# Performance work log

Measured on AMD Instinct MI355X. Metric: run time of the kernel, lower is better.

Reference implementation:

```python
import jax, jax.numpy as jnp
import numpy as np

N = 100000      # nodes
E = 400000      # edges (before self loops)
D_ATOM = 98
D_BOND = 13
EMB = 128
HEADS = 4
L = 4           # num_layer


def prelu(x, a):
    return jnp.where(x >= 0, x, a * x)


def setup_inputs() -> dict:
    key = jax.random.key(0)
    ks = jax.random.split(key, 12)
    s = 0.05
    inp = {
        "x": jax.random.normal(ks[0], (N, D_ATOM), dtype=jnp.float32),
        "edge_index": jax.random.randint(ks[1], (2, E), 0, N, dtype=jnp.int64),
        "edge_attr": jax.random.uniform(ks[2], (E, D_BOND), dtype=jnp.float32),
        # GNN-level params
        "x_emb_W": jax.random.normal(ks[3], (D_ATOM, EMB), dtype=jnp.float32) * s,
        "prelu_gnn": jnp.float32(0.25),
        # per-layer GATConv params, stacked on leading layer axis
        "wl_W": jax.random.normal(ks[4], (L, EMB, HEADS * EMB), dtype=jnp.float32) * s,
        "wl_b": jnp.zeros((L, HEADS * EMB), dtype=jnp.float32),
        "att": jax.random.normal(ks[5], (L, HEADS, 2 * EMB), dtype=jnp.float32) * s,
        "gat_bias": jnp.zeros((L, EMB), dtype=jnp.float32),
        "ee_W": jax.random.normal(ks[6], (L, D_BOND, HEADS * EMB), dtype=jnp.float32) * s,
        "ee_b": jnp.zeros((L, HEADS * EMB), dtype=jnp.float32),
        "prelu_gat": jnp.full((L,), 0.25, dtype=jnp.float32),
        # LayerNorm params per layer
        "ln_g": jnp.ones((L, EMB), dtype=jnp.float32),
        "ln_b": jnp.zeros((L, EMB), dtype=jnp.float32),
    }
    return inp


def reference(x, edge_index, edge_attr, x_emb_W, prelu_gnn, wl_W, wl_b, att,
              gat_bias, ee_W, ee_b, prelu_gat, ln_g, ln_b):
    # add self loops: (i, i) for every node; self-loop edge_attr = zeros
    loop = jnp.arange(N, dtype=edge_index.dtype)
    src = jnp.concatenate([edge_index[0], loop])  # [E+N] source (j)
    dst = jnp.concatenate([edge_index[1], loop])  # [E+N] target (i)
    ea = jnp.concatenate(
        [edge_attr, jnp.zeros((N, D_BOND), dtype=edge_attr.dtype)], axis=0)

    # input embedding + shared PReLU
    h = prelu(x @ x_emb_W, prelu_gnn)  # [N, EMB]

    for l in range(L):
        a = prelu_gat[l]
        ee = prelu(ea @ ee_W[l] + ee_b[l], a)       # [E+N, H*EMB]
        xw = prelu(h @ wl_W[l] + wl_b[l], a)        # [N, H*EMB]
        x_i = xw[dst].reshape(-1, HEADS, EMB)       # target feats
        x_j = (xw[src] + ee).reshape(-1, HEADS, EMB)  # source feats + edge emb
        # attention logits: cat([x_i,x_j]) . att
        alpha = (x_i * att[l, :, :EMB]).sum(-1) + (x_j * att[l, :, EMB:]).sum(-1)
        alpha = prelu(alpha, a)                     # [E+N, HEADS]
        # segment softmax grouped by src (edge_index[0]), as in the module
        m = jax.ops.segment_max(alpha, src, num_segments=N)
        alpha = jnp.exp(alpha - m[src])
        ssum = jax.ops.segment_sum(alpha, src, num_segments=N)
        alpha = alpha / (ssum[src] + 1e-16)
        # weighted messages, scatter-add to target nodes
        msg = (x_j * alpha[:, :, None]).reshape(-1, HEADS * EMB)
        aggr = jax.ops.segment_sum(msg, dst, num_segments=N)
        aggr = aggr.reshape(N, HEADS, EMB).mean(axis=1) + gat_bias[l]
        # LayerNorm
        mu = aggr.mean(-1, keepdims=True)
        var = ((aggr - mu) ** 2).mean(-1, keepdims=True)
        hn = (aggr - mu) / jnp.sqrt(var + 1e-5) * ln_g[l] + ln_b[l]
        # dropout is identity (drop_ratio=0); PReLU on all but last layer
        h = hn if l == L - 1 else prelu(hn, prelu_gnn)

    return h  # JK='last'
```

## Files before the change

kernel.cpp:

```cpp
#include <hip/hip_runtime.h>
#include <stdint.h>

#define NN 100000
#define NE 400000
#define NT 500000
#define DA 98
#define DB 13
#define EMB 128
#define HE 512
#define NWAVE 8192
#define IMSK 0x0FFFFFFF

typedef unsigned short ushort_t;
typedef __bf16 bf16x8 __attribute__((ext_vector_type(8)));
typedef float floatx4 __attribute__((ext_vector_type(4)));
typedef __fp16 fp16v2 __attribute__((ext_vector_type(2)));

__device__ __forceinline__ float prelu_f(float x, float a) { return x >= 0.f ? x : a * x; }

__device__ __forceinline__ ushort_t f2bf(float f) {
    unsigned u = __float_as_uint(f);
    unsigned r = (u + 0x7fffu + ((u >> 16) & 1u)) >> 16;
    return (ushort_t)r;
}
__device__ __forceinline__ float bflo(unsigned u) { return __uint_as_float(u << 16); }
__device__ __forceinline__ float bfhi(unsigned u) { return __uint_as_float(u & 0xffff0000u); }

__device__ __forceinline__ float dot2(unsigned a, unsigned b, float c) {
    return __builtin_amdgcn_fdot2(__builtin_bit_cast(fp16v2, a), __builtin_bit_cast(fp16v2, b), c, false);
}

__device__ __forceinline__ unsigned pk2(float lo, float hi) {
    fp16v2 p = __builtin_amdgcn_cvt_pkrtz(lo, hi);
    return __builtin_bit_cast(unsigned, p);
}

__global__ void k_count(const int* __restrict__ ei, int* __restrict__ sc, int* __restrict__ dc) {
    int e = blockIdx.x * 256 + threadIdx.x;
    if (e >= NT) return;
    int s, d;
    if (e < NE) { s = ei[e]; d = ei[NE + e]; } else { s = d = e - NE; }
    atomicAdd(sc + s, 1);
    atomicAdd(dc + d, 1);
}

__global__ void k_scan1(const int* __restrict__ cnt, int* __restrict__ part, int* __restrict__ bsum) {
    __shared__ int tmp[512];
    int t = threadIdx.x, i = blockIdx.x * 512 + t;
    int v = (i < NN) ? cnt[i] : 0;
    tmp[t] = v;
    __syncthreads();
    for (int off = 1; off < 512; off <<= 1) {
        int x = (t >= off) ? tmp[t - off] : 0;
        __syncthreads();
        tmp[t] += x;
        __syncthreads();
    }
    if (i < NN) part[i] = tmp[t] - v;
    if (t == 511) bsum[blockIdx.x] = tmp[t];
}

__global__ void k_scan2(int* __restrict__ bsum, int nb) {
    __shared__ int tmp[256];
    int t = threadIdx.x;
    int v = (t < nb) ? bsum[t] : 0;
    tmp[t] = v;
    __syncthreads();
    for (int off = 1; off < 256; off <<= 1) {
        int x = (t >= off) ? tmp[t - off] : 0;
        __syncthreads();
        tmp[t] += x;
        __syncthreads();
    }
    if (t < nb) bsum[t] = tmp[t] - v;
}

__global__ void k_scan3(const int* __restrict__ part, const int* __restrict__ bsum,
                        int* __restrict__ off, int* __restrict__ cur) {
    int i = blockIdx.x * 256 + threadIdx.x;
    if (i < NN) {
        int v = part[i] + bsum[i >> 9];
        off[i] = v;
        cur[i] = v;
    }
    if (i == 0) off[NN] = NT;
}

__global__ void k_fill(const int* __restrict__ ei, int* __restrict__ scur, int* __restrict__ dcur,
                       int* __restrict__ seid, int* __restrict__ deid, int* __restrict__ s2p) {
    int e = blockIdx.x * 256 + threadIdx.x;
    if (e >= NT) return;
    int s, d;
    if (e < NE) { s = ei[e]; d = ei[NE + e]; } else { s = d = e - NE; }
    int p = atomicAdd(scur + s, 1);
    seid[p] = e;
    s2p[e] = p;
    deid[atomicAdd(dcur + d, 1)] = e;
}

__global__ void k_wrange2(const int* __restrict__ doff, const int* __restrict__ soff,
                          int* __restrict__ nstart, int* __restrict__ nstart_s) {
    int w = blockIdx.x * 256 + threadIdx.x;
    if (w > NWAVE) return;
    long long target = (long long)w * NT / NWAVE;
    int lo = 0, hi = NN;
    while (lo < hi) {
        int mid = (lo + hi) >> 1;
        if ((long long)doff[mid] < target) lo = mid + 1; else hi = mid;
    }
    nstart[w] = lo;
    lo = 0; hi = NN;
    while (lo < hi) {
        int mid = (lo + hi) >> 1;
        if ((long long)soff[mid] < target) lo = mid + 1; else hi = mid;
    }
    nstart_s[w] = lo;
}

__global__ void k_dprep(const int* __restrict__ deid, const int* __restrict__ ei,
                        const float* __restrict__ ea, const int* __restrict__ s2p,
                        int2* __restrict__ sd_d, unsigned* __restrict__ ea_d) {
    int i = blockIdx.x * 256 + threadIdx.x;
    if (i >= NT + 4) return;
    unsigned p[8] = {0, 0, 0, 0, 0, 0, 0, 0};
    int s = 0, pos = 0;
    if (i < NT) {
        int eid = deid[i];
        if (eid < NE) {
            s = ei[eid];
            float v[DB];
            #pragma unroll
            for (int k = 0; k < DB; ++k) v[k] = ea[(size_t)eid * DB + k];
            #pragma unroll
            for (int kp = 0; kp < 6; ++kp) p[kp] = pk2(v[2 * kp], v[2 * kp + 1]);
            p[6] = pk2(v[12], 0.f);
        } else {
            s = (eid - NE) | (1 << 30);
        }
        pos = s2p[eid];
    }
    uint4* o = (uint4*)&ea_d[(size_t)i * 8];
    o[0] = make_uint4(p[0], p[1], p[2], p[3]);
    o[1] = make_uint4(p[4], p[5], p[6], p[7]);
    sd_d[i] = make_int2(s, pos);
}

__global__ void k_sprep(const int* __restrict__ seid, const int* __restrict__ ei,
                        const float* __restrict__ ea,
                        int* __restrict__ dst_s, unsigned* __restrict__ ea_s) {
    int i = blockIdx.x * 256 + threadIdx.x;
    if (i >= NT + 4) return;
    unsigned p[8] = {0, 0, 0, 0, 0, 0, 0, 0};
    int d = 0;
    if (i < NT) {
        int eid = seid[i];
        if (eid < NE) {
            d = ei[NE + eid];
            float v[DB];
            #pragma unroll
            for (int k = 0; k < DB; ++k) v[k] = ea[(size_t)eid * DB + k];
            #pragma unroll
            for (int kp = 0; kp < 6; ++kp) p[kp] = pk2(v[2 * kp], v[2 * kp + 1]);
            p[6] = pk2(v[12], 0.f);
        } else {
            d = (eid - NE) | (1 << 30);
        }
    }
    uint4* o = (uint4*)&ea_s[(size_t)i * 8];
    o[0] = make_uint4(p[0], p[1], p[2], p[3]);
    o[1] = make_uint4(p[4], p[5], p[6], p[7]);
    dst_s[i] = d;
}

__global__ void k_prep_all(const float* __restrict__ x, const float* __restrict__ xembW,
                           const float* __restrict__ wlW, const float* __restrict__ eeW,
                           ushort_t* __restrict__ xb, ushort_t* __restrict__ Wxt,
                           ushort_t* __restrict__ Wtg, unsigned* __restrict__ eeWp) {
    int idx = blockIdx.x * 256 + threadIdx.x;
    if (idx < NN * 128) {
        int col = idx & 127, n = idx >> 7;
        float v = (col < DA) ? x[(size_t)n * DA + col] : 0.f;
        xb[idx] = f2bf(v);
        return;
    }
    idx -= NN * 128;
    if (idx < 128 * 128) {
        int k = idx & 127, n = idx >> 7;
        float v = (k < DA) ? xembW[(size_t)k * EMB + n] : 0.f;
        Wxt[idx] = f2bf(v);
        return;
    }
    idx -= 128 * 128;
    if (idx < 4 * 512 * 128) {
        int k = idx & 127;
        int n = (idx >> 7) & 511;
        int l = idx >> 16;
        Wtg[idx] = f2bf(wlW[(size_t)l * 65536 + k * 512 + n]);
        return;
    }
    idx -= 4 * 512 * 128;
    if (idx < 4 * 7 * 512) {
        int l = idx / 3584;
        int rem = idx - l * 3584;
        int kp = rem >> 9;
        int ch = rem & 511;
        float lo = eeW[((size_t)l * DB + 2 * kp) * HE + ch];
        float hi = (2 * kp + 1 < DB) ? eeW[((size_t)l * DB + 2 * kp + 1) * HE + ch] : 0.f;
        eeWp[idx] = pk2(lo, hi);
    }
}
#define PREP_TOTAL (NN * 128 + 128 * 128 + 4 * 512 * 128 + 4 * 7 * 512)

__global__ __launch_bounds__(256) void k_embed_m(const ushort_t* __restrict__ xb, const ushort_t* __restrict__ Wxt,
                                                 const float* __restrict__ pg, ushort_t* __restrict__ hb) {
    __shared__ ushort_t At[64 * 136];
    __shared__ ushort_t Bt[128 * 136];
    int t = threadIdx.x;
    int m0 = blockIdx.x * 64;
    for (int idx = t; idx < 64 * 16; idx += 256) {
        int r = idx >> 4, co = (idx & 15) * 8;
        int gr = m0 + r; if (gr >= NN) gr = 0;
        *(uint4*)&At[r * 136 + co] = *(const uint4*)&xb[(size_t)gr * 128 + co];
    }
    for (int idx = t; idx < 128 * 16; idx += 256) {
        int n = idx >> 4, ko = (idx & 15) * 8;
        *(uint4*)&Bt[n * 136 + ko] = *(const uint4*)&Wxt[n * 128 + ko];
    }
    float p = pg[0];
    __syncthreads();

    int wv = t >> 6, lane = t & 63;
    int ml = lane & 15, kq = lane >> 4;
    int n0w = wv * 32;
    floatx4 acc[4][2];
    #pragma unroll
    for (int mt = 0; mt < 4; ++mt)
        #pragma unroll
        for (int nt = 0; nt < 2; ++nt)
            acc[mt][nt] = (floatx4){0.f, 0.f, 0.f, 0.f};

    #pragma unroll
    for (int k0 = 0; k0 < 128; k0 += 32) {
        bf16x8 af[4], bfv[2];
        #pragma unroll
        for (int mt = 0; mt < 4; ++mt) {
            uint4 u = *(const uint4*)&At[(mt * 16 + ml) * 136 + k0 + kq * 8];
            af[mt] = __builtin_bit_cast(bf16x8, u);
        }
        #pragma unroll
        for (int nt = 0; nt < 2; ++nt) {
            uint4 u = *(const uint4*)&Bt[(n0w + nt * 16 + ml) * 136 + k0 + kq * 8];
            bfv[nt] = __builtin_bit_cast(bf16x8, u);
        }
        #pragma unroll
        for (int mt = 0; mt < 4; ++mt)
            #pragma unroll
            for (int nt = 0; nt < 2; ++nt)
                acc[mt][nt] = __builtin_amdgcn_mfma_f32_16x16x32_bf16(af[mt], bfv[nt], acc[mt][nt], 0, 0, 0);
    }
    #pragma unroll
    for (int nt = 0; nt < 2; ++nt) {
        int col = n0w + nt * 16 + ml;
        #pragma unroll
        for (int mt = 0; mt < 4; ++mt) {
            int row = m0 + mt * 16 + kq * 4;
            #pragma unroll
            for (int q = 0; q < 4; ++q) {
                int r = row + q;
                if (r < NN) hb[(size_t)r * EMB + col] = f2bf(prelu_f(acc[mt][nt][q], p));
            }
        }
    }
}

__global__ __launch_bounds__(256) void k_gemm(const ushort_t* __restrict__ hb, const ushort_t* __restrict__ Wtg,
                                              const float* __restrict__ bl, const float* __restrict__ pa,
                                              const float* __restrict__ attl,
                                              ushort_t* __restrict__ xw,
                                              float* __restrict__ ddst, float* __restrict__ dsrc) {
    __shared__ ushort_t At[64 * 136];
    __shared__ ushort_t Bt[128 * 136];
    int t = threadIdx.x;
    int m0 = blockIdx.x * 64;
    int h = blockIdx.y;
    int n0 = h * 128;
    for (int idx = t; idx < 64 * 16; idx += 256) {
        int r = idx >> 4, co = (idx & 15) * 8;
        int gr = m0 + r; if (gr >= NN) gr = 0;
        *(uint4*)&At[r * 136 + co] = *(const uint4*)&hb[(size_t)gr * EMB + co];
    }
    for (int idx = t; idx < 128 * 16; idx += 256) {
        int n = idx >> 4, ko = (idx & 15) * 8;
        *(uint4*)&Bt[n * 136 + ko] = *(const uint4*)&Wtg[(size_t)(n0 + n) * 128 + ko];
    }
    float a = pa[0];
    __syncthreads();

    int wv = t >> 6, lane = t & 63;
    int ml = lane & 15, kq = lane >> 4;
    int n0w = wv * 32;
    floatx4 acc[4][2];
    #pragma unroll
    for (int mt = 0; mt < 4; ++mt)
        #pragma unroll
        for (int nt = 0; nt < 2; ++nt)
            acc[mt][nt] = (floatx4){0.f, 0.f, 0.f, 0.f};

    #pragma unroll
    for (int k0 = 0; k0 < 128; k0 += 32) {
        bf16x8 af[4], bfv[2];
        #pragma unroll
        for (int mt = 0; mt < 4; ++mt) {
            uint4 u = *(const uint4*)&At[(mt * 16 + ml) * 136 + k0 + kq * 8];
            af[mt] = __builtin_bit_cast(bf16x8, u);
        }
        #pragma unroll
        for (int nt = 0; nt < 2; ++nt) {
            uint4 u = *(const uint4*)&Bt[(n0w + nt * 16 + ml) * 136 + k0 + kq * 8];
            bfv[nt] = __builtin_bit_cast(bf16x8, u);
        }
        #pragma unroll
        for (int mt = 0; mt < 4; ++mt)
            #pragma unroll
            for (int nt = 0; nt < 2; ++nt)
                acc[mt][nt] = __builtin_amdgcn_mfma_f32_16x16x32_bf16(af[mt], bfv[nt], acc[mt][nt], 0, 0, 0);
    }
    __syncthreads();
    float* sdd = (float*)At;
    float* sds = (float*)At + 256;

    float pd[4][4], ps[4][4];
    #pragma unroll
    for (int mt = 0; mt < 4; ++mt)
        #pragma unroll
        for (int q = 0; q < 4; ++q) { pd[mt][q] = 0.f; ps[mt][q] = 0.f; }

    #pragma unroll
    for (int nt = 0; nt < 2; ++nt) {
        int ch = n0w + nt * 16 + ml;
        int col = n0 + ch;
        float bv = bl[col];
        float a1v = attl[h * 256 + ch];
        float a2v = attl[h * 256 + 128 + ch];
        #pragma unroll
        for (int mt = 0; mt < 4; ++mt) {
            int row = m0 + mt * 16 + kq * 4;
            #pragma unroll
            for (int q = 0; q < 4; ++q) {
                int r = row + q;
                float v = prelu_f(acc[mt][nt][q] + bv, a);
                if (r < NN) xw[(size_t)r * HE + col] = f2bf(v);
                pd[mt][q] += v * a1v;
                ps[mt][q] += v * a2v;
            }
        }
    }
    #pragma unroll
    for (int mt = 0; mt < 4; ++mt)
        #pragma unroll
        for (int q = 0; q < 4; ++q) {
            float d = pd[mt][q], s = ps[mt][q];
            #pragma unroll
            for (int m = 1; m < 16; m <<= 1) {
                d += __shfl_xor(d, m, 64);
                s += __shfl_xor(s, m, 64);
            }
            if (ml == 0) {
                int lr = mt * 16 + kq * 4 + q;
                sdd[wv * 64 + lr] = d;
                sds[wv * 64 + lr] = s;
            }
        }
    __syncthreads();
    if (t < 64) {
        int r = m0 + t;
        if (r < NN) {
            float d = sdd[t] + sdd[64 + t] + sdd[128 + t] + sdd[192 + t];
            float s = sds[t] + sds[64 + t] + sds[128 + t] + sds[192 + t];
            ddst[r * 4 + h] = d;
            dsrc[r * 4 + h] = s;
        }
    }
}

__global__ __launch_bounds__(256) void k_edgesm(const int* __restrict__ nstart_s,
                                                const int* __restrict__ soff,
                                                const unsigned* __restrict__ ea_s,
                                                const int* __restrict__ dst_s,
                                                const unsigned* __restrict__ eeWp, const float* __restrict__ ebl,
                                                const float* __restrict__ attl, const float* __restrict__ pa,
                                                const float* __restrict__ ddst, const float* __restrict__ dsrc,
                                                float* __restrict__ alpha_s) {
    int t = threadIdx.x;
    float a = pa[0];
    int lane = t & 63;
    int w = blockIdx.x * 4 + (t >> 6);
    int hd = lane >> 4;
    int cm = (lane & 15) * 8;
    int c0 = lane * 8;
    uint4 wpa[7], wpb[7];
    #pragma unroll
    for (int kp = 0; kp < 7; ++kp) {
        wpa[kp] = *(const uint4*)&eeWp[kp * HE + c0];
        wpb[kp] = *(const uint4*)&eeWp[kp * HE + c0 + 4];
    }
    float a2[8], eb[8];
    #pragma unroll
    for (int q = 0; q < 8; ++q) {
        a2[q] = attl[hd * 256 + 128 + cm + q];
        eb[q] = ebl[c0 + q];
    }
    float pselfR = 0.f;
    #pragma unroll
    for (int q = 0; q < 8; ++q) pselfR += prelu_f(eb[q], a) * a2[q];
    #pragma unroll
    for (int m = 1; m < 16; m <<= 1) pselfR += __shfl_xor(pselfR, m, 64);

    int head = lane & 3;
    int slot = lane >> 2;

    int n0 = nstart_s[w], n1 = nstart_s[w + 1];
    if (n0 >= n1) return;
    int e0 = soff[n0], e1 = soff[n1];

    uint4 eaAa = *(const uint4*)&ea_s[(size_t)e0 * 8];
    uint4 eaAb = *(const uint4*)&ea_s[(size_t)e0 * 8 + 4];
    int rA = dst_s[e0], rB = dst_s[e0 + 1];
    int dA = rA & IMSK, fA = rA >> 30;
    int dB = rB & IMSK, fB = rB >> 30;
    float diA = ddst[dA * 4 + hd];

    int n = n0;
    int b = e0;
    int bEnd = soff[n0 + 1];
    bool small = (bEnd - b) <= 16;
    float sj = dsrc[n * 4 + hd];
    float mx = -1e30f;
    float myLg = -1e30f;

    for (int i = e0; i < e1; ++i) {
        uint4 eaNa = *(const uint4*)&ea_s[(size_t)(i + 1) * 8];
        uint4 eaNb = *(const uint4*)&ea_s[(size_t)(i + 1) * 8 + 4];
        int rC = dst_s[i + 2];
        int dC = rC & IMSK, fC = rC >> 30;
        float diB = ddst[dB * 4 + hd];
        float p;
        if (__builtin_amdgcn_readfirstlane(fA)) {
            p = pselfR;
        } else {
            unsigned ec[7] = {eaAa.x, eaAa.y, eaAa.z, eaAa.w, eaAb.x, eaAb.y, eaAb.z};
            float v[8];
            #pragma unroll
            for (int q = 0; q < 8; ++q) v[q] = eb[q];
            #pragma unroll
            for (int kp = 0; kp < 7; ++kp) {
                v[0] = dot2(ec[kp], wpa[kp].x, v[0]);
                v[1] = dot2(ec[kp], wpa[kp].y, v[1]);
                v[2] = dot2(ec[kp], wpa[kp].z, v[2]);
                v[3] = dot2(ec[kp], wpa[kp].w, v[3]);
                v[4] = dot2(ec[kp], wpb[kp].x, v[4]);
                v[5] = dot2(ec[kp], wpb[kp].y, v[5]);
                v[6] = dot2(ec[kp], wpb[kp].z, v[6]);
                v[7] = dot2(ec[kp], wpb[kp].w, v[7]);
            }
            p = 0.f;
            #pragma unroll
            for (int q = 0; q < 8; ++q) p += prelu_f(v[q], a) * a2[q];
            #pragma unroll
            for (int m = 1; m < 16; m <<= 1) p += __shfl_xor(p, m, 64);
        }
        float lg = prelu_f(diA + sj + p, a);
        if (small) {
            float lgH = __shfl(lg, head * 16, 64);
            myLg = (slot == (i - b)) ? lgH : myLg;
        } else {
            if ((lane & 15) == 0) {
                alpha_s[(size_t)i * 4 + hd] = lg;
                mx = fmaxf(mx, lg);
            }
        }
        if (i + 1 == bEnd) {
            if (small) {
                float mh = myLg;
                #pragma unroll
                for (int m = 4; m < 64; m <<= 1) mh = fmaxf(mh, __shfl_xor(mh, m, 64));
                float ex = __expf(myLg - mh);
                float s = ex;
                #pragma unroll
                for (int m = 4; m < 64; m <<= 1) s += __shfl_xor(s, m, 64);
                float inv = 1.f / (s + 1e-16f);
                if (slot < bEnd - b)
                    alpha_s[(size_t)(b + slot) * 4 + head] = ex * inv;
            } else {
                float m0v = __shfl(mx, 0, 64), m1v = __shfl(mx, 16, 64),
                      m2v = __shfl(mx, 32, 64), m3v = __shfl(mx, 48, 64);
                float mh = head == 0 ? m0v : head == 1 ? m1v : head == 2 ? m2v : m3v;
                asm volatile("s_waitcnt vmcnt(0)" ::: "memory");
                float s = 0.f;
                for (int idx = b + (lane >> 2); idx < bEnd; idx += 16) {
                    float x = alpha_s[(size_t)idx * 4 + head];
                    float ex = __expf(x - mh);
                    s += ex;
                    alpha_s[(size_t)idx * 4 + head] = ex;
                }
                #pragma unroll
                for (int m = 4; m < 64; m <<= 1) s += __shfl_xor(s, m, 64);
                float inv = 1.f / (s + 1e-16f);
                asm volatile("s_waitcnt vmcnt(0)" ::: "memory");
                for (int idx = b + (lane >> 2); idx < bEnd; idx += 16)
                    alpha_s[(size_t)idx * 4 + head] *= inv;
            }
            ++n;
            if (i + 1 < e1) {
                b = bEnd;
                bEnd = soff[n + 1];
                small = (bEnd - b) <= 16;
                sj = dsrc[n * 4 + hd];
                mx = -1e30f;
                myLg = -1e30f;
            }
        }
        eaAa = eaNa; eaAb = eaNb;
        dA = dB; fA = fB;
        dB = dC; fB = fC;
        diA = diB;
    }
}

__global__ __launch_bounds__(256) void k_aggr(const int* __restrict__ nstart,
                                              const int* __restrict__ doff,
                                              const int2* __restrict__ sd_d,
                                              const unsigned* __restrict__ ea_d,
                                              const unsigned* __restrict__ eeWp, const float* __restrict__ ebl,
                                              const float* __restrict__ pa, const ushort_t* __restrict__ xw,
                                              const float* __restrict__ alpha_s,
                                              const float* __restrict__ gbias, const float* __restrict__ lng,
                                              const float* __restrict__ lnb, const float* __restrict__ pgnn,
                                              int last, ushort_t* __restrict__ hb_out, float* __restrict__ fout) {
    int t = threadIdx.x;
    float a = pa[0], pg = pgnn[0];
    int lane = t & 63;
    int w = blockIdx.x * 4 + (t >> 6);
    int hd = lane >> 4;
    int cm = (lane & 15) * 8;
    int c0 = lane * 8;
    uint4 wpa[7], wpb[7];
    #pragma unroll
    for (int kp = 0; kp < 7; ++kp) {
        wpa[kp] = *(const uint4*)&eeWp[kp * HE + c0];
        wpb[kp] = *(const uint4*)&eeWp[kp * HE + c0 + 4];
    }
    float eb[8], ebp[8];
    #pragma unroll
    for (int q = 0; q < 8; ++q) {
        eb[q] = ebl[c0 + q];
        ebp[q] = prelu_f(eb[q], a);
    }
    float gbv[8], gv[8], bbv[8];
    *(float4*)&gbv[0] = *(const float4*)&gbias[cm];
    *(float4*)&gbv[4] = *(const float4*)&gbias[cm + 4];
    *(float4*)&gv[0]  = *(const float4*)&lng[cm];
    *(float4*)&gv[4]  = *(const float4*)&lng[cm + 4];
    *(float4*)&bbv[0] = *(const float4*)&lnb[cm];
    *(float4*)&bbv[4] = *(const float4*)&lnb[cm + 4];

    int n0 = nstart[w], n1 = nstart[w + 1];
    if (n0 >= n1) return;
    int e0 = doff[n0];
    int e1 = doff[n1];

    int2 rA = sd_d[e0], rB = sd_d[e0 + 1], rN = sd_d[e0 + 2];
    int sA = rA.x & IMSK, fA = rA.x >> 30, pA = rA.y;
    int sB = rB.x & IMSK, fB = rB.x >> 30, pB = rB.y;
    int sN = rN.x & IMSK, fN = rN.x >> 30, pN = rN.y;
    uint4 xwA = *(const uint4*)&xw[(size_t)sA * HE + c0];
    float alA = alpha_s[(size_t)pA * 4 + hd];
    uint4 xwB = *(const uint4*)&xw[(size_t)sB * HE + c0];
    float alB = alpha_s[(size_t)pB * 4 + hd];
    uint4 eaCa = *(const uint4*)&ea_d[(size_t)e0 * 8];
    uint4 eaCb = *(const uint4*)&ea_d[(size_t)e0 * 8 + 4];

    int n = n0;
    int b1 = doff[n0 + 1];
    int nn2 = (n0 + 2 <= NN) ? n0 + 2 : NN;
    int b2 = doff[nn2];
    float acc[8] = {0.f, 0.f, 0.f, 0.f, 0.f, 0.f, 0.f, 0.f};

    for (int i = e0; i < e1; ++i) {
        uint4 eaNa = *(const uint4*)&ea_d[(size_t)(i + 1) * 8];
        uint4 eaNb = *(const uint4*)&ea_d[(size_t)(i + 1) * 8 + 4];
        uint4 xwC = *(const uint4*)&xw[(size_t)sN * HE + c0];
        float alC = alpha_s[(size_t)pN * 4 + hd];
        int2 rN2 = sd_d[i + 3];
        int sN2 = rN2.x & IMSK, fN2 = rN2.x >> 30, pN2 = rN2.y;
        float pw[8];
        if (__builtin_amdgcn_readfirstlane(fA)) {
            #pragma unroll
            for (int q = 0; q < 8; ++q) pw[q] = ebp[q];
        } else {
            unsigned ec[7] = {eaCa.x, eaCa.y, eaCa.z, eaCa.w, eaCb.x, eaCb.y, eaCb.z};
            float wv[8];
            #pragma unroll
            for (int q = 0; q < 8; ++q) wv[q] = eb[q];
            #pragma unroll
            for (int kp = 0; kp < 7; ++kp) {
                wv[0] = dot2(ec[kp], wpa[kp].x, wv[0]);
                wv[1] = dot2(ec[kp], wpa[kp].y, wv[1]);
                wv[2] = dot2(ec[kp], wpa[kp].z, wv[2]);
                wv[3] = dot2(ec[kp], wpa[kp].w, wv[3]);
                wv[4] = dot2(ec[kp], wpb[kp].x, wv[4]);
                wv[5] = dot2(ec[kp], wpb[kp].y, wv[5]);
                wv[6] = dot2(ec[kp], wpb[kp].z, wv[6]);
                wv[7] = dot2(ec[kp], wpb[kp].w, wv[7]);
            }
            #pragma unroll
            for (int q = 0; q < 8; ++q) pw[q] = prelu_f(wv[q], a);
        }
        float xv[8] = {bflo(xwA.x), bfhi(xwA.x), bflo(xwA.y), bfhi(xwA.y),
                       bflo(xwA.z), bfhi(xwA.z), bflo(xwA.w), bfhi(xwA.w)};
        #pragma unroll
        for (int q = 0; q < 8; ++q) acc[q] += (xv[q] + pw[q]) * alA;
        if (i + 1 == b1) {
            float hm[8];
            #pragma unroll
            for (int q = 0; q < 8; ++q) {
                float v = acc[q];
                v += __shfl_xor(v, 16, 64);
                v += __shfl_xor(v, 32, 64);
                hm[q] = 0.25f * v + gbv[q];
            }
            float s8 = 0.f, q8 = 0.f;
            #pragma unroll
            for (int q = 0; q < 8; ++q) { s8 += hm[q]; q8 += hm[q] * hm[q]; }
            #pragma unroll
            for (int m = 1; m < 16; m <<= 1) {
                s8 += __shfl_xor(s8, m, 64);
                q8 += __shfl_xor(q8, m, 64);
            }
            float mu = s8 * (1.f / 128.f);
            float var = q8 * (1.f / 128.f) - mu * mu;
            float rstd = rsqrtf(var + 1e-5f);
            if (lane < 16) {
                float o[8];
                #pragma unroll
                for (int q = 0; q < 8; ++q) {
                    float v = (hm[q] - mu) * rstd * gv[q] + bbv[q];
                    o[q] = last ? v : prelu_f(v, pg);
                }
                if (last) {
                    float4* op = (float4*)&fout[(size_t)n * EMB + lane * 8];
                    op[0] = make_float4(o[0], o[1], o[2], o[3]);
                    op[1] = make_float4(o[4], o[5], o[6], o[7]);
                } else {
                    uint4 ob;
                    ob.x = (unsigned)f2bf(o[0]) | ((unsigned)f2bf(o[1]) << 16);
                    ob.y = (unsigned)f2bf(o[2]) | ((unsigned)f2bf(o[3]) << 16);
                    ob.z = (unsigned)f2bf(o[4]) | ((unsigned)f2bf(o[5]) << 16);
                    ob.w = (unsigned)f2bf(o[6]) | ((unsigned)f2bf(o[7]) << 16);
                    *(uint4*)&hb_out[(size_t)n * EMB + lane * 8] = ob;
                }
            }
            #pragma unroll
            for (int q = 0; q < 8; ++q) acc[q] = 0.f;
            ++n;
            b1 = b2;
            int nx = (n + 2 <= NN) ? n + 2 : NN;
            b2 = doff[nx];
        }
        xwA = xwB; alA = alB;
        xwB = xwC; alB = alC;
        sN = sN2; pN = pN2;
        fA = fB; fB = fN; fN = fN2;
        eaCa = eaNa; eaCb = eaNb;
    }
}

extern "C" void kernel_launch(void* const* d_in, const int* in_sizes, int n_in,
                              void* d_out, int out_size, void* d_ws, size_t ws_size,
                              hipStream_t stream) {
    const float* x     = (const float*)d_in[0];
    const int*   ei    = (const int*)d_in[1];
    const float* ea    = (const float*)d_in[2];
    const float* xembW = (const float*)d_in[3];
    const float* pgnn  = (const float*)d_in[4];
    const float* wlW   = (const float*)d_in[5];
    const float* wlb   = (const float*)d_in[6];
    const float* att   = (const float*)d_in[7];
    const float* gbias = (const float*)d_in[8];
    const float* eeW   = (const float*)d_in[9];
    const float* eeb   = (const float*)d_in[10];
    const float* pgat  = (const float*)d_in[11];
    const float* lng   = (const float*)d_in[12];
    const float* lnb   = (const float*)d_in[13];

    char* w = (char*)d_ws;
    size_t off = 0;
    auto alloc = [&](size_t nbytes) -> char* {
        char* p = w + off;
        off += (nbytes + 255) & ~(size_t)255;
        return p;
    };
    ushort_t* hb    = (ushort_t*)alloc((size_t)NN * EMB * 2);
    ushort_t* xw    = (ushort_t*)alloc((size_t)NN * HE * 2);
    ushort_t* Wtg   = (ushort_t*)alloc((size_t)4 * 512 * 128 * 2);
    ushort_t* Wxt   = (ushort_t*)alloc((size_t)128 * 128 * 2);
    unsigned* eeWp  = (unsigned*)alloc((size_t)4 * 7 * 512 * 4);
    float*    ddst  = (float*)alloc((size_t)NN * 4 * 4);
    float*    dsrc  = (float*)alloc((size_t)NN * 4 * 4);
    float*    alpha = (float*)alloc((size_t)NT * 4 * 4);
    unsigned* ea_d  = (unsigned*)alloc((size_t)(NT + 4) * 8 * 4);
    unsigned* ea_s  = (unsigned*)alloc((size_t)(NT + 4) * 8 * 4);
    int2* sd_d    = (int2*)alloc((size_t)(NT + 4) * 8);
    int* cnt2     = (int*)alloc((size_t)2 * NN * 4);
    int* scnt     = cnt2;
    int* dcnt     = cnt2 + NN;
    int* soff     = (int*)alloc((size_t)(NN + 1) * 4);
    int* doff     = (int*)alloc((size_t)(NN + 1) * 4);
    int* scur     = (int*)alloc((size_t)NN * 4);
    int* dcur     = (int*)alloc((size_t)NN * 4);
    int* seid     = (int*)alloc((size_t)NT * 4);
    int* deid     = (int*)alloc((size_t)NT * 4);
    int* s2p      = (int*)alloc((size_t)NT * 4);
    int* dst_s    = (int*)alloc((size_t)(NT + 4) * 4);
    int* nstart   = (int*)alloc((size_t)(NWAVE + 1) * 4);
    int* nstart_s = (int*)alloc((size_t)(NWAVE + 1) * 4);
    int* part     = (int*)alloc((size_t)NN * 4);
    int* bsum     = (int*)alloc(256 * 4);

    ushort_t* xb = xw;

    hipMemsetAsync(cnt2, 0, (size_t)2 * NN * 4, stream);
    k_count<<<(NT + 255) / 256, 256, 0, stream>>>(ei, scnt, dcnt);
    k_scan1<<<196, 512, 0, stream>>>(scnt, part, bsum);
    k_scan2<<<1, 256, 0, stream>>>(bsum, 196);
    k_scan3<<<391, 256, 0, stream>>>(part, bsum, soff, scur);
    k_scan1<<<196, 512, 0, stream>>>(dcnt, part, bsum);
    k_scan2<<<1, 256, 0, stream>>>(bsum, 196);
    k_scan3<<<391, 256, 0, stream>>>(part, bsum, doff, dcur);
    k_fill<<<(NT + 255) / 256, 256, 0, stream>>>(ei, scur, dcur, seid, deid, s2p);
    k_wrange2<<<(NWAVE + 1 + 255) / 256, 256, 0, stream>>>(doff, soff, nstart, nstart_s);
    k_dprep<<<(NT + 4 + 255) / 256, 256, 0, stream>>>(deid, ei, ea, s2p, sd_d, ea_d);
    k_sprep<<<(NT + 4 + 255) / 256, 256, 0, stream>>>(seid, ei, ea, dst_s, ea_s);
    k_prep_all<<<(PREP_TOTAL + 255) / 256, 256, 0, stream>>>(x, xembW, wlW, eeW, xb, Wxt, Wtg, eeWp);
    k_embed_m<<<(NN + 63) / 64, 256, 0, stream>>>(xb, Wxt, pgnn, hb);

    for (int l = 0; l < 4; ++l) {
        const float* bl  = wlb + (size_t)l * HE;
        const float* al  = att + (size_t)l * 1024;
        const unsigned* eWl = eeWp + (size_t)l * 7 * HE;
        const float* ebl = eeb + (size_t)l * HE;
        const float* pa  = pgat + l;
        const ushort_t* Wt = Wtg + (size_t)l * 512 * 128;
        k_gemm<<<dim3((NN + 63) / 64, 4), 256, 0, stream>>>(hb, Wt, bl, pa, al, xw, ddst, dsrc);
        k_edgesm<<<2048, 256, 0, stream>>>(nstart_s, soff, ea_s, dst_s, eWl, ebl, al, pa,
                                           ddst, dsrc, alpha);
        k_aggr<<<2048, 256, 0, stream>>>(nstart, doff, sd_d, ea_d, eWl, ebl, pa, xw, alpha,
                                         gbias + (size_t)l * EMB, lng + (size_t)l * EMB,
                                         lnb + (size_t)l * EMB, pgnn, (l == 3) ? 1 : 0,
                                         hb, (float*)d_out);
    }
}
```

Measured before the change: 1.747 ms.

## Handle self-loops implicitly instead of materializing them as CSR edges

Self-loop edges are no longer stored in the src/dst CSR arrays. Each node's self term is computed directly: a known logit in the softmax kernel, and an extra weighted term added when the aggregation kernel finishes a node. This removes the per-edge flag checks and the divergent branch, and cuts the prep arrays and edge-stream traffic from NE+N to NE entries. The cost is more complex offset arithmetic (offsets minus node index) and extra loops for nodes with no real edges, which could unbalance the per-wave work split.

Measured after the change: 1.781 ms. About the same (+1.9%).

```diff
diff --git a/kernel.cpp b/kernel.cpp
--- a/kernel.cpp
+++ b/kernel.cpp
@@ -9,7 +9,6 @@
 #define EMB 128
 #define HE 512
 #define NWAVE 8192
-#define IMSK 0x0FFFFFFF
 
 typedef unsigned short ushort_t;
 typedef __bf16 bf16x8 __attribute__((ext_vector_type(8)));
@@ -81,63 +80,58 @@
     if (i < NN) {
         int v = part[i] + bsum[i >> 9];
         off[i] = v;
-        cur[i] = v;
+        cur[i] = v - i;
     }
     if (i == 0) off[NN] = NT;
 }
 
-__global__ void k_fill(const int* __restrict__ ei, int* __restrict__ scur, int* __restrict__ dcur,
-                       int* __restrict__ seid, int* __restrict__ deid, int* __restrict__ s2p) {
+__global__ void k_fill(const int* __restrict__ ei, int* __restrict__ scur2, int* __restrict__ dcur2,
+                       int* __restrict__ seid2, int* __restrict__ deid2, int* __restrict__ s2p_full) {
     int e = blockIdx.x * 256 + threadIdx.x;
-    if (e >= NT) return;
-    int s, d;
-    if (e < NE) { s = ei[e]; d = ei[NE + e]; } else { s = d = e - NE; }
-    int p = atomicAdd(scur + s, 1);
-    seid[p] = e;
-    s2p[e] = p;
-    deid[atomicAdd(dcur + d, 1)] = e;
+    if (e >= NE) return;
+    int s = ei[e], d = ei[NE + e];
+    int cs = atomicAdd(scur2 + s, 1);
+    seid2[cs] = e;
+    s2p_full[e] = cs + s + 1;
+    deid2[atomicAdd(dcur2 + d, 1)] = e;
 }
 
 __global__ void k_wrange2(const int* __restrict__ doff, const int* __restrict__ soff,
                           int* __restrict__ nstart, int* __restrict__ nstart_s) {
     int w = blockIdx.x * 256 + threadIdx.x;
     if (w > NWAVE) return;
-    long long target = (long long)w * NT / NWAVE;
+    long long target = (long long)w * NE / NWAVE;
     int lo = 0, hi = NN;
     while (lo < hi) {
         int mid = (lo + hi) >> 1;
-        if ((long long)doff[mid] < target) lo = mid + 1; else hi = mid;
+        if ((long long)(doff[mid] - mid) < target) lo = mid + 1; else hi = mid;
     }
     nstart[w] = lo;
     lo = 0; hi = NN;
     while (lo < hi) {
         int mid = (lo + hi) >> 1;
-        if ((long long)soff[mid] < target) lo = mid + 1; else hi = mid;
+        if ((long long)(soff[mid] - mid) < target) lo = mid + 1; else hi = mid;
     }
     nstart_s[w] = lo;
 }
 
-__global__ void k_dprep(const int* __restrict__ deid, const int* __restrict__ ei,
-                        const float* __restrict__ ea, const int* __restrict__ s2p,
+__global__ void k_dprep(const int* __restrict__ deid2, const int* __restrict__ ei,
+                        const float* __restrict__ ea, const int* __restrict__ s2p_full,
                         int2* __restrict__ sd_d, unsigned* __restrict__ ea_d) {
     int i = blockIdx.x * 256 + threadIdx.x;
-    if (i >= NT + 4) return;
+    if (i >= NE + 4) return;
     unsigned p[8] = {0, 0, 0, 0, 0, 0, 0, 0};
     int s = 0, pos = 0;
-    if (i < NT) {
-        int eid = deid[i];
-        if (eid < NE) {
-            s = ei[eid];
-            float v[DB];
-            #pragma unroll
-            for (int k = 0; k < DB; ++k) v[k] = ea[(size_t)eid * DB + k];
-            #pragma unroll
-            for (int kp = 0; kp < 6; ++kp) p[kp] = pk2(v[2 * kp], v[2 * kp + 1]);
-            p[6] = pk2(v[12], 0.f);
-        } else {
-            s = (eid - NE) | (1 << 30);
-        }
-        pos = s2p[eid];
+    if (i < NE) {
+        int eid = deid2[i];
+        s = ei[eid];
+        pos = s2p_full[eid];
+        float v[DB];
+        #pragma unroll
+        for (int k = 0; k < DB; ++k) v[k] = ea[(size_t)eid * DB + k];
+        #pragma unroll
+        for (int kp = 0; kp < 6; ++kp) p[kp] = pk2(v[2 * kp], v[2 * kp + 1]);
+        p[6] = pk2(v[12], 0.f);
     }
     uint4* o = (uint4*)&ea_d[(size_t)i * 8];
     o[0] = make_uint4(p[0], p[1], p[2], p[3]);
@@ -145,26 +139,22 @@
     sd_d[i] = make_int2(s, pos);
 }
 
-__global__ void k_sprep(const int* __restrict__ seid, const int* __restrict__ ei,
+__global__ void k_sprep(const int* __restrict__ seid2, const int* __restrict__ ei,
                         const float* __restrict__ ea,
                         int* __restrict__ dst_s, unsigned* __restrict__ ea_s) {
     int i = blockIdx.x * 256 + threadIdx.x;
-    if (i >= NT + 4) return;
+    if (i >= NE + 4) return;
     unsigned p[8] = {0, 0, 0, 0, 0, 0, 0, 0};
     int d = 0;
-    if (i < NT) {
-        int eid = seid[i];
-        if (eid < NE) {
-            d = ei[NE + eid];
-            float v[DB];
-            #pragma unroll
-            for (int k = 0; k < DB; ++k) v[k] = ea[(size_t)eid * DB + k];
-            #pragma unroll
-            for (int kp = 0; kp < 6; ++kp) p[kp] = pk2(v[2 * kp], v[2 * kp + 1]);
-            p[6] = pk2(v[12], 0.f);
-        } else {
-            d = (eid - NE) | (1 << 30);
-        }
+    if (i < NE) {
+        int eid = seid2[i];
+        d = ei[NE + eid];
+        float v[DB];
+        #pragma unroll
+        for (int k = 0; k < DB; ++k) v[k] = ea[(size_t)eid * DB + k];
+        #pragma unroll
+        for (int kp = 0; kp < 6; ++kp) p[kp] = pk2(v[2 * kp], v[2 * kp + 1]);
+        p[6] = pk2(v[12], 0.f);
     }
     uint4* o = (uint4*)&ea_s[(size_t)i * 8];
     o[0] = make_uint4(p[0], p[1], p[2], p[3]);
@@ -421,65 +411,71 @@
 
     int n0 = nstart_s[w], n1 = nstart_s[w + 1];
     if (n0 >= n1) return;
-    int e0 = soff[n0], e1 = soff[n1];
+    int e0 = soff[n0] - n0;
+    int e1 = soff[n1] - n1;
+
+    int n = n0;
+    int sBase = soff[n0];
+    while (n < n1) {
+        int nbq = soff[n + 1];
+        if (nbq - (n + 1) != e0) break;
+        if ((lane & 15) == 0) alpha_s[(size_t)sBase * 4 + hd] = 1.0f;
+        sBase = nbq; ++n;
+    }
+    if (e0 >= e1) return;
 
     uint4 eaAa = *(const uint4*)&ea_s[(size_t)e0 * 8];
     uint4 eaAb = *(const uint4*)&ea_s[(size_t)e0 * 8 + 4];
-    int rA = dst_s[e0], rB = dst_s[e0 + 1];
-    int dA = rA & IMSK, fA = rA >> 30;
-    int dB = rB & IMSK, fB = rB >> 30;
+    int dA = dst_s[e0], dB = dst_s[e0 + 1];
     float diA = ddst[dA * 4 + hd];
 
-    int n = n0;
+    int nb = soff[n + 1];
+    int bEnd = nb - (n + 1);
     int b = e0;
-    int bEnd = soff[n0 + 1];
-    bool small = (bEnd - b) <= 16;
+    bool small = (nb - sBase) <= 16;
     float sj = dsrc[n * 4 + hd];
-    float mx = -1e30f;
-    float myLg = -1e30f;
+    float diSelf = ddst[n * 4 + hd];
+    float lgSelf = prelu_f(diSelf + sj + pselfR, a);
+    float mx = lgSelf;
+    float myLg;
+    { float lgSH = __shfl(lgSelf, head * 16, 64); myLg = (slot == 0) ? lgSH : -1e30f; }
+    if (!small && (lane & 15) == 0) alpha_s[(size_t)sBase * 4 + hd] = lgSelf;
 
     for (int i = e0; i < e1; ++i) {
         uint4 eaNa = *(const uint4*)&ea_s[(size_t)(i + 1) * 8];
         uint4 eaNb = *(const uint4*)&ea_s[(size_t)(i + 1) * 8 + 4];
-        int rC = dst_s[i + 2];
-        int dC = rC & IMSK, fC = rC >> 30;
+        int dC = dst_s[i + 2];
         float diB = ddst[dB * 4 + hd];
-        float p;
-        if (__builtin_amdgcn_readfirstlane(fA)) {
-            p = pselfR;
-        } else {
-            unsigned ec[7] = {eaAa.x, eaAa.y, eaAa.z, eaAa.w, eaAb.x, eaAb.y, eaAb.z};
-            float v[8];
-            #pragma unroll
-            for (int q = 0; q < 8; ++q) v[q] = eb[q];
-            #pragma unroll
-            for (int kp = 0; kp < 7; ++kp) {
-                v[0] = dot2(ec[kp], wpa[kp].x, v[0]);
-                v[1] = dot2(ec[kp], wpa[kp].y, v[1]);
-                v[2] = dot2(ec[kp], wpa[kp].z, v[2]);
-                v[3] = dot2(ec[kp], wpa[kp].w, v[3]);
-                v[4] = dot2(ec[kp], wpb[kp].x, v[4]);
-                v[5] = dot2(ec[kp], wpb[kp].y, v[5]);
-                v[6] = dot2(ec[kp], wpb[kp].z, v[6]);
-                v[7] = dot2(ec[kp], wpb[kp].w, v[7]);
-            }
-            p = 0.f;
-            #pragma unroll
-            for (int q = 0; q < 8; ++q) p += prelu_f(v[q], a) * a2[q];
-            #pragma unroll
-            for (int m = 1; m < 16; m <<= 1) p += __shfl_xor(p, m, 64);
-        }
+        unsigned ec[7] = {eaAa.x, eaAa.y, eaAa.z, eaAa.w, eaAb.x, eaAb.y, eaAb.z};
+        float v[8];
+        #pragma unroll
+        for (int q = 0; q < 8; ++q) v[q] = eb[q];
+        #pragma unroll
+        for (int kp = 0; kp < 7; ++kp) {
+            v[0] = dot2(ec[kp], wpa[kp].x, v[0]);
+            v[1] = dot2(ec[kp], wpa[kp].y, v[1]);
+            v[2] = dot2(ec[kp], wpa[kp].z, v[2]);
+            v[3] = dot2(ec[kp], wpa[kp].w, v[3]);
+            v[4] = dot2(ec[kp], wpb[kp].x, v[4]);
+            v[5] = dot2(ec[kp], wpb[kp].y, v[5]);
+            v[6] = dot2(ec[kp], wpb[kp].z, v[6]);
+            v[7] = dot2(ec[kp], wpb[kp].w, v[7]);
+        }
+        float p = 0.f;
+        #pragma unroll
+        for (int q = 0; q < 8; ++q) p += prelu_f(v[q], a) * a2[q];
+        #pragma unroll
+        for (int m = 1; m < 16; m <<= 1) p += __shfl_xor(p, m, 64);
         float lg = prelu_f(diA + sj + p, a);
         if (small) {
             float lgH = __shfl(lg, head * 16, 64);
-            myLg = (slot == (i - b)) ? lgH : myLg;
-        } else {
-            if ((lane & 15) == 0) {
-                alpha_s[(size_t)i * 4 + hd] = lg;
-                mx = fmaxf(mx, lg);
-            }
+            myLg = (slot == (i - b) + 1) ? lgH : myLg;
+        } else if ((lane & 15) == 0) {
+            alpha_s[(size_t)(sBase + 1 + (i - b)) * 4 + hd] = lg;
+            mx = fmaxf(mx, lg);
         }
         if (i + 1 == bEnd) {
+            int degF = nb - sBase;
             if (small) {
                 float mh = myLg;
                 #pragma unroll
@@ -489,15 +485,15 @@
                 #pragma unroll
                 for (int m = 4; m < 64; m <<= 1) s += __shfl_xor(s, m, 64);
                 float inv = 1.f / (s + 1e-16f);
-                if (slot < bEnd - b)
-                    alpha_s[(size_t)(b + slot) * 4 + head] = ex * inv;
+                if (slot < degF)
+                    alpha_s[(size_t)(sBase + slot) * 4 + head] = ex * inv;
             } else {
                 float m0v = __shfl(mx, 0, 64), m1v = __shfl(mx, 16, 64),
                       m2v = __shfl(mx, 32, 64), m3v = __shfl(mx, 48, 64);
                 float mh = head == 0 ? m0v : head == 1 ? m1v : head == 2 ? m2v : m3v;
                 asm volatile("s_waitcnt vmcnt(0)" ::: "memory");
                 float s = 0.f;
-                for (int idx = b + (lane >> 2); idx < bEnd; idx += 16) {
+                for (int idx = sBase + (lane >> 2); idx < nb; idx += 16) {
                     float x = alpha_s[(size_t)idx * 4 + head];
                     float ex = __expf(x - mh);
                     s += ex;
@@ -507,28 +503,38 @@
                 for (int m = 4; m < 64; m <<= 1) s += __shfl_xor(s, m, 64);
                 float inv = 1.f / (s + 1e-16f);
                 asm volatile("s_waitcnt vmcnt(0)" ::: "memory");
-                for (int idx = b + (lane >> 2); idx < bEnd; idx += 16)
+                for (int idx = sBase + (lane >> 2); idx < nb; idx += 16)
                     alpha_s[(size_t)idx * 4 + head] *= inv;
             }
-            ++n;
+            ++n; sBase = nb;
+            while (n < n1) {
+                int nbq = soff[n + 1];
+                if (nbq - (n + 1) != i + 1) break;
+                if ((lane & 15) == 0) alpha_s[(size_t)sBase * 4 + hd] = 1.0f;
+                sBase = nbq; ++n;
+            }
             if (i + 1 < e1) {
-                b = bEnd;
-                bEnd = soff[n + 1];
-                small = (bEnd - b) <= 16;
+                nb = soff[n + 1];
+                bEnd = nb - (n + 1);
+                b = i + 1;
+                small = (nb - sBase) <= 16;
                 sj = dsrc[n * 4 + hd];
-                mx = -1e30f;
-                myLg = -1e30f;
+                diSelf = ddst[n * 4 + hd];
+                lgSelf = prelu_f(diSelf + sj + pselfR, a);
+                mx = lgSelf;
+                float lgSH = __shfl(lgSelf, head * 16, 64);
+                myLg = (slot == 0) ? lgSH : -1e30f;
+                if (!small && (lane & 15) == 0) alpha_s[(size_t)sBase * 4 + hd] = lgSelf;
             }
         }
         eaAa = eaNa; eaAb = eaNb;
-        dA = dB; fA = fB;
-        dB = dC; fB = fC;
+        dA = dB; dB = dC;
         diA = diB;
     }
 }
 
 __global__ __launch_bounds__(256) void k_aggr(const int* __restrict__ nstart,
-                                              const int* __restrict__ doff,
+                                              const int* __restrict__ doff, const int* __restrict__ soff,
                                               const int2* __restrict__ sd_d,
                                               const unsigned* __restrict__ ea_d,
                                               const unsigned* __restrict__ eeWp, const float* __restrict__ ebl,
@@ -564,26 +570,82 @@
     *(float4*)&bbv[0] = *(const float4*)&lnb[cm];
     *(float4*)&bbv[4] = *(const float4*)&lnb[cm + 4];
 
+    auto finishNode = [&](int node, const float* accp, uint4 xwS, float alS) {
+        float xvS[8] = {bflo(xwS.x), bfhi(xwS.x), bflo(xwS.y), bfhi(xwS.y),
+                        bflo(xwS.z), bfhi(xwS.z), bflo(xwS.w), bfhi(xwS.w)};
+        float hm[8];
+        #pragma unroll
+        for (int q = 0; q < 8; ++q) {
+            float v = accp[q] + (xvS[q] + ebp[q]) * alS;
+            v += __shfl_xor(v, 16, 64);
+            v += __shfl_xor(v, 32, 64);
+            hm[q] = 0.25f * v + gbv[q];
+        }
+        float s8 = 0.f, q8 = 0.f;
+        #pragma unroll
+        for (int q = 0; q < 8; ++q) { s8 += hm[q]; q8 += hm[q] * hm[q]; }
+        #pragma unroll
+        for (int m = 1; m < 16; m <<= 1) {
+            s8 += __shfl_xor(s8, m, 64);
+            q8 += __shfl_xor(q8, m, 64);
+        }
+        float mu = s8 * (1.f / 128.f);
+        float var = q8 * (1.f / 128.f) - mu * mu;
+        float rstd = rsqrtf(var + 1e-5f);
+        if (lane < 16) {
+            float o[8];
+            #pragma unroll
+            for (int q = 0; q < 8; ++q) {
+                float vv = (hm[q] - mu) * rstd * gv[q] + bbv[q];
+                o[q] = last ? vv : prelu_f(vv, pg);
+            }
+            if (last) {
+                float4* op = (float4*)&fout[(size_t)node * EMB + lane * 8];
+                op[0] = make_float4(o[0], o[1], o[2], o[3]);
+                op[1] = make_float4(o[4], o[5], o[6], o[7]);
+            } else {
+                uint4 ob;
+                ob.x = (unsigned)f2bf(o[0]) | ((unsigned)f2bf(o[1]) << 16);
+                ob.y = (unsigned)f2bf(o[2]) | ((unsigned)f2bf(o[3]) << 16);
+                ob.z = (unsigned)f2bf(o[4]) | ((unsigned)f2bf(o[5]) << 16);
+                ob.w = (unsigned)f2bf(o[6]) | ((unsigned)f2bf(o[7]) << 16);
+                *(uint4*)&hb_out[(size_t)node * EMB + lane * 8] = ob;
+            }
+        }
+    };
+
     int n0 = nstart[w], n1 = nstart[w + 1];
     if (n0 >= n1) return;
-    int e0 = doff[n0];
-    int e1 = doff[n1];
+    int e0 = doff[n0] - n0;
+    int e1 = doff[n1] - n1;
+    int n = n0;
+    const float accz[8] = {0.f, 0.f, 0.f, 0.f, 0.f, 0.f, 0.f, 0.f};
+
+    while (n < n1) {
+        int db = doff[n + 1];
+        if (db - (n + 1) != e0) break;
+        int so = soff[n];
+        uint4 xwS = *(const uint4*)&xw[(size_t)n * HE + c0];
+        float alS = alpha_s[(size_t)so * 4 + hd];
+        finishNode(n, accz, xwS, alS);
+        ++n;
+    }
+    if (e0 >= e1) return;
 
     int2 rA = sd_d[e0], rB = sd_d[e0 + 1], rN = sd_d[e0 + 2];
-    int sA = rA.x & IMSK, fA = rA.x >> 30, pA = rA.y;
-    int sB = rB.x & IMSK, fB = rB.x >> 30, pB = rB.y;
-    int sN = rN.x & IMSK, fN = rN.x >> 30, pN = rN.y;
+    int sA = rA.x, pA = rA.y;
+    int sB = rB.x, pB = rB.y;
+    int sN = rN.x, pN = rN.y;
     uint4 xwA = *(const uint4*)&xw[(size_t)sA * HE + c0];
     float alA = alpha_s[(size_t)pA * 4 + hd];
     uint4 xwB = *(const uint4*)&xw[(size_t)sB * HE + c0];
     float alB = alpha_s[(size_t)pB * 4 + hd];
     uint4 eaCa = *(const uint4*)&ea_d[(size_t)e0 * 8];
     uint4 eaCb = *(const uint4*)&ea_d[(size_t)e0 * 8 + 4];
-
-    int n = n0;
-    int b1 = doff[n0 + 1];
-    int nn2 = (n0 + 2 <= NN) ? n0 + 2 : NN;
-    int b2 = doff[nn2];
+    uint4 xwSelfA = *(const uint4*)&xw[(size_t)n * HE + c0];
+    float alSelfA = alpha_s[(size_t)soff[n] * 4 + hd];
+
+    int b1 = doff[n + 1] - (n + 1);
     float acc[8] = {0.f, 0.f, 0.f, 0.f, 0.f, 0.f, 0.f, 0.f};
 
     for (int i = e0; i < e1; ++i) {
@@ -592,85 +654,49 @@
         uint4 xwC = *(const uint4*)&xw[(size_t)sN * HE + c0];
         float alC = alpha_s[(size_t)pN * 4 + hd];
         int2 rN2 = sd_d[i + 3];
-        int sN2 = rN2.x & IMSK, fN2 = rN2.x >> 30, pN2 = rN2.y;
-        float pw[8];
-        if (__builtin_amdgcn_readfirstlane(fA)) {
-            #pragma unroll
-            for (int q = 0; q < 8; ++q) pw[q] = ebp[q];
-        } else {
-            unsigned ec[7] = {eaCa.x, eaCa.y, eaCa.z, eaCa.w, eaCb.x, eaCb.y, eaCb.z};
-            float wv[8];
-            #pragma unroll
-            for (int q = 0; q < 8; ++q) wv[q] = eb[q];
-            #pragma unroll
-            for (int kp = 0; kp < 7; ++kp) {
-                wv[0] = dot2(ec[kp], wpa[kp].x, wv[0]);
-                wv[1] = dot2(ec[kp], wpa[kp].y, wv[1]);
-                wv[2] = dot2(ec[kp], wpa[kp].z, wv[2]);
-                wv[3] = dot2(ec[kp], wpa[kp].w, wv[3]);
-                wv[4] = dot2(ec[kp], wpb[kp].x, wv[4]);
-                wv[5] = dot2(ec[kp], wpb[kp].y, wv[5]);
-                wv[6] = dot2(ec[kp], wpb[kp].z, wv[6]);
-                wv[7] = dot2(ec[kp], wpb[kp].w, wv[7]);
-            }
-            #pragma unroll
-            for (int q = 0; q < 8; ++q) pw[q] = prelu_f(wv[q], a);
+        unsigned ec[7] = {eaCa.x, eaCa.y, eaCa.z, eaCa.w, eaCb.x, eaCb.y, eaCb.z};
+        float wv[8];
+        #pragma unroll
+        for (int q = 0; q < 8; ++q) wv[q] = eb[q];
+        #pragma unroll
+        for (int kp = 0; kp < 7; ++kp) {
+            wv[0] = dot2(ec[kp], wpa[kp].x, wv[0]);
+            wv[1] = dot2(ec[kp], wpa[kp].y, wv[1]);
+            wv[2] = dot2(ec[kp], wpa[kp].z, wv[2]);
+            wv[3] = dot2(ec[kp], wpa[kp].w, wv[3]);
+            wv[4] = dot2(ec[kp], wpb[kp].x, wv[4]);
+            wv[5] = dot2(ec[kp], wpb[kp].y, wv[5]);
+            wv[6] = dot2(ec[kp], wpb[kp].z, wv[6]);
+            wv[7] = dot2(ec[kp], wpb[kp].w, wv[7]);
         }
         float xv[8] = {bflo(xwA.x), bfhi(xwA.x), bflo(xwA.y), bfhi(xwA.y),
                        bflo(xwA.z), bfhi(xwA.z), bflo(xwA.w), bfhi(xwA.w)};
         #pragma unroll
-        for (int q = 0; q < 8; ++q) acc[q] += (xv[q] + pw[q]) * alA;
+        for (int q = 0; q < 8; ++q) acc[q] += (xv[q] + prelu_f(wv[q], a)) * alA;
         if (i + 1 == b1) {
-            float hm[8];
-            #pragma unroll
-            for (int q = 0; q < 8; ++q) {
-                float v = acc[q];
-                v += __shfl_xor(v, 16, 64);
-                v += __shfl_xor(v, 32, 64);
-                hm[q] = 0.25f * v + gbv[q];
-            }
-            float s8 = 0.f, q8 = 0.f;
-            #pragma unroll
-            for (int q = 0; q < 8; ++q) { s8 += hm[q]; q8 += hm[q] * hm[q]; }
-            #pragma unroll
-            for (int m = 1; m < 16; m <<= 1) {
-                s8 += __shfl_xor(s8, m, 64);
-                q8 += __shfl_xor(q8, m, 64);
-            }
-            float mu = s8 * (1.f / 128.f);
-            float var = q8 * (1.f / 128.f) - mu * mu;
-            float rstd = rsqrtf(var + 1e-5f);
-            if (lane < 16) {
-                float o[8];
-                #pragma unroll
-                for (int q = 0; q < 8; ++q) {
-                    float v = (hm[q] - mu) * rstd * gv[q] + bbv[q];
-                    o[q] = last ? v : prelu_f(v, pg);
-                }
-                if (last) {
-                    float4* op = (float4*)&fout[(size_t)n * EMB + lane * 8];
-                    op[0] = make_float4(o[0], o[1], o[2], o[3]);
-                    op[1] = make_float4(o[4], o[5], o[6], o[7]);
-                } else {
-                    uint4 ob;
-                    ob.x = (unsigned)f2bf(o[0]) | ((unsigned)f2bf(o[1]) << 16);
-                    ob.y = (unsigned)f2bf(o[2]) | ((unsigned)f2bf(o[3]) << 16);
-                    ob.z = (unsigned)f2bf(o[4]) | ((unsigned)f2bf(o[5]) << 16);
-                    ob.w = (unsigned)f2bf(o[6]) | ((unsigned)f2bf(o[7]) << 16);
-                    *(uint4*)&hb_out[(size_t)n * EMB + lane * 8] = ob;
-                }
-            }
+            finishNode(n, acc, xwSelfA, alSelfA);
             #pragma unroll
             for (int q = 0; q < 8; ++q) acc[q] = 0.f;
             ++n;
-            b1 = b2;
-            int nx = (n + 2 <= NN) ? n + 2 : NN;
-            b2 = doff[nx];
+            while (n < n1) {
+                int db = doff[n + 1];
+                if (db - (n + 1) != i + 1) break;
+                int so = soff[n];
+                uint4 xwS = *(const uint4*)&xw[(size_t)n * HE + c0];
+                float alS = alpha_s[(size_t)so * 4 + hd];
+                finishNode(n, accz, xwS, alS);
+                ++n;
+            }
+            if (i + 1 < e1) {
+                b1 = doff[n + 1] - (n + 1);
+                int so = soff[n];
+                xwSelfA = *(const uint4*)&xw[(size_t)n * HE + c0];
+                alSelfA = alpha_s[(size_t)so * 4 + hd];
+            }
         }
         xwA = xwB; alA = alB;
         xwB = xwC; alB = alC;
-        sN = sN2; pN = pN2;
-        fA = fB; fB = fN; fN = fN2;
+        sN = rN2.x; pN = rN2.y;
         eaCa = eaNa; eaCb = eaNb;
     }
 }
@@ -708,9 +734,9 @@
     float*    ddst  = (float*)alloc((size_t)NN * 4 * 4);
     float*    dsrc  = (float*)alloc((size_t)NN * 4 * 4);
     float*    alpha = (float*)alloc((size_t)NT * 4 * 4);
-    unsigned* ea_d  = (unsigned*)alloc((size_t)(NT + 4) * 8 * 4);
-    unsigned* ea_s  = (unsigned*)alloc((size_t)(NT + 4) * 8 * 4);
-    int2* sd_d    = (int2*)alloc((size_t)(NT + 4) * 8);
+    unsigned* ea_d  = (unsigned*)alloc((size_t)(NE + 4) * 8 * 4);
+    unsigned* ea_s  = (unsigned*)alloc((size_t)(NE + 4) * 8 * 4);
+    int2* sd_d    = (int2*)alloc((size_t)(NE + 4) * 8);
     int* cnt2     = (int*)alloc((size_t)2 * NN * 4);
     int* scnt     = cnt2;
     int* dcnt     = cnt2 + NN;
@@ -718,10 +744,10 @@
     int* doff     = (int*)alloc((size_t)(NN + 1) * 4);
     int* scur     = (int*)alloc((size_t)NN * 4);
     int* dcur     = (int*)alloc((size_t)NN * 4);
-    int* seid     = (int*)alloc((size_t)NT * 4);
-    int* deid     = (int*)alloc((size_t)NT * 4);
-    int* s2p      = (int*)alloc((size_t)NT * 4);
-    int* dst_s    = (int*)alloc((size_t)(NT + 4) * 4);
+    int* seid2    = (int*)alloc((size_t)NE * 4);
+    int* deid2    = (int*)alloc((size_t)NE * 4);
+    int* s2p      = (int*)alloc((size_t)NE * 4);
+    int* dst_s    = (int*)alloc((size_t)(NE + 4) * 4);
     int* nstart   = (int*)alloc((size_t)(NWAVE + 1) * 4);
     int* nstart_s = (int*)alloc((size_t)(NWAVE + 1) * 4);
     int* part     = (int*)alloc((size_t)NN * 4);
@@ -737,10 +763,10 @@
     k_scan1<<<196, 512, 0, stream>>>(dcnt, part, bsum);
     k_scan2<<<1, 256, 0, stream>>>(bsum, 196);
     k_scan3<<<391, 256, 0, stream>>>(part, bsum, doff, dcur);
-    k_fill<<<(NT + 255) / 256, 256, 0, stream>>>(ei, scur, dcur, seid, deid, s2p);
+    k_fill<<<(NE + 255) / 256, 256, 0, stream>>>(ei, scur, dcur, seid2, deid2, s2p);
     k_wrange2<<<(NWAVE + 1 + 255) / 256, 256, 0, stream>>>(doff, soff, nstart, nstart_s);
-    k_dprep<<<(NT + 4 + 255) / 256, 256, 0, stream>>>(deid, ei, ea, s2p, sd_d, ea_d);
-    k_sprep<<<(NT + 4 + 255) / 256, 256, 0, stream>>>(seid, ei, ea, dst_s, ea_s);
+    k_dprep<<<(NE + 4 + 255) / 256, 256, 0, stream>>>(deid2, ei, ea, s2p, sd_d, ea_d);
+    k_sprep<<<(NE + 4 + 255) / 256, 256, 0, stream>>>(seid2, ei, ea, dst_s, ea_s);
     k_prep_all<<<(PREP_TOTAL + 255) / 256, 256, 0, stream>>>(x, xembW, wlW, eeW, xb, Wxt, Wtg, eeWp);
     k_embed_m<<<(NN + 63) / 64, 256, 0, stream>>>(xb, Wxt, pgnn, hb);
 
@@ -754,7 +780,7 @@
         k_gemm<<<dim3((NN + 63) / 64, 4), 256, 0, stream>>>(hb, Wt, bl, pa, al, xw, ddst, dsrc);
         k_edgesm<<<2048, 256, 0, stream>>>(nstart_s, soff, ea_s, dst_s, eWl, ebl, al, pa,
                                            ddst, dsrc, alpha);
-        k_aggr<<<2048, 256, 0, stream>>>(nstart, doff, sd_d, ea_d, eWl, ebl, pa, xw, alpha,
+        k_aggr<<<2048, 256, 0, stream>>>(nstart, doff, soff, sd_d, ea_d, eWl, ebl, pa, xw, alpha,
                                          gbias + (size_t)l * EMB, lng + (size_t)l * EMB,
                                          lnb + (size_t)l * EMB, pgnn, (l == 3) ? 1 : 0,
                                          hb, (float*)d_out);
```
